# Kernel tuning notes

Hardware: AMD Instinct MI355X
Metric: run time of the kernel (lower is better)

Reference implementation:

```python
import jax, jax.numpy as jnp
import numpy as np

DIMS = [1024, 1024, 1024, 512]
BATCH = 1024
BETA = 1e-3
N_ITER = 20
LR_STATE = 0.5


def setup_inputs() -> dict:
    key = jax.random.key(0)
    ks = jax.random.split(key, 2 + len(DIMS) - 1)
    x = jax.random.normal(ks[0], (BATCH, DIMS[0]), dtype=jnp.float32)
    y = jax.random.normal(ks[1], (BATCH, DIMS[-1]), dtype=jnp.float32)
    inp = {"x": x, "y": y}
    # Weights: torch used randn*0.1; at these dims that makes the lr_state=0.5
    # gradient relaxation numerically unstable (Hessian I + W W^T has spectral
    # norm >> 2). We use a spectrally-normalized scale 0.5/sqrt(d_in) so the
    # fixed-point iteration is stable; the math of the module is unchanged.
    for i, (d_in, d_out) in enumerate(zip(DIMS[:-1], DIMS[1:])):
        inp[f"W{i}"] = jax.random.normal(ks[2 + i], (d_in, d_out), dtype=jnp.float32) * (0.5 / np.sqrt(d_in))
    return inp


def _forward_chain(x, Ws):
    # states[k+1] = states[k] @ W_k  -> the exact fixed point of the free energy
    states = [x]
    for W in Ws:
        states.append(states[-1] @ W)
    return states


def _state_grads(states, Ws, beta, y, coupled):
    """dE/ds_k for k=1..L (E = 0.5*sum ||s_{k+1} - s_k W_k||^2 + beta*0.5||s_L - y||^2).

    coupled=True reproduces torch's FIRST relaxation step, where states[1:]
    are still graph-connected via s_{k+1} = s_k @ W_k, so gradients also flow
    along that chain (g_total[k] = g_direct[k] + g_total[k+1] @ W_k^T).
    Later steps treat states as detached leaves (direct partials only).
    """
    L = len(Ws)
    g = []
    for k in range(1, L + 1):
        gk = states[k] - states[k - 1] @ Ws[k - 1]          # target side of term k-1
        if k < L:
            gk = gk - (states[k + 1] - states[k] @ Ws[k]) @ Ws[k].T  # pred side of term k
        else:
            gk = gk + beta * (states[k] - y)                 # clamp term
        g.append(gk)
    if coupled:
        for i in range(L - 2, -1, -1):
            g[i] = g[i] + g[i + 1] @ Ws[i + 1].T
    return g


def _relax_clamped(x, y, Ws, beta, n_iter, lr):
    states = _forward_chain(x, Ws)
    for it in range(n_iter):
        g = _state_grads(states, Ws, beta, y, coupled=(it == 0))
        states = [states[0]] + [s - lr * gk for s, gk in zip(states[1:], g)]
    return states


def _weight_grads(states, Ws):
    # dE/dW_i = s_i^T (s_i W_i - s_{i+1})
    return [states[i].T @ (states[i] @ W - states[i + 1]) for i, W in enumerate(Ws)]


def reference(x, y, W0, W1, W2):
    Ws = [W0, W1, W2]
    # Free phase (beta=0): the initial chain is the exact fixed point -- every
    # residual s_{k+1} - s_k W_k is bitwise zero, so all 20 torch relaxation
    # steps are exact no-ops. s0 is therefore just the forward chain.
    s0 = _forward_chain(x, Ws)
    # Weakly clamped phase.
    sb = _relax_clamped(x, y, Ws, BETA, N_ITER, LR_STATE)
    g0 = _weight_grads(s0, Ws)   # exactly zero at the free fixed point
    gb = _weight_grads(sb, Ws)
    ep_grads = [(b - a) / BETA for b, a in zip(gb, g0)]
    loss = jnp.mean((s0[-1] - y) ** 2)
    # Flatten EP weight grads + scalar loss into one vector output.
    return jnp.concatenate([g.ravel() for g in ep_grads] + [loss[None]])
```

## Files before the change

### kernel.cpp

```cpp
#include <hip/hip_runtime.h>


typedef float f32x4 __attribute__((ext_vector_type(4)));
typedef __bf16 bf16x8 __attribute__((ext_vector_type(8)));
typedef unsigned short u16;
typedef unsigned int u32;

namespace {

constexpr float LR = 0.5f;
constexpr float BETA = 1e-3f;

__device__ inline void splitbf(float v, u16& h, u16& l) {
  __bf16 hb = (__bf16)v;
  float hf = (float)hb;
  __bf16 lb = (__bf16)(v - hf);
  h = __builtin_bit_cast(u16, hb);
  l = __builtin_bit_cast(u16, lb);
}
__device__ inline u32 pack2(u16 a, u16 b) { return (u32)a | ((u32)b << 16); }

__device__ inline f32x4 MF(bf16x8 a, bf16x8 b, f32x4 c) {
  return __builtin_amdgcn_mfma_f32_16x16x32_bf16(a, b, c, 0, 0, 0);
}

__device__ inline int swzc(int row, int col) {
  return (col & ~63) | ((((col >> 3) & 7) ^ (row & 7)) << 3) | (col & 7);
}

struct GemmP {
  const u16 *Ah, *Al, *Bh, *Bl;
  const float *E0, *E1;
  float *of, *of2, *of3;
  u16 *oh, *ol;
  float alpha, c0, c1v;
  int N, K, ntn, role;
};

template <int NP>
__global__ __launch_bounds__(256) void gemm_g(GemmP ca, GemmP cb, GemmP cc,
                                              int nb0, int nb01) {
  constexpr int NARR = NP + 1;
  constexpr int NCH = NARR * 2;
  __shared__ u16 lds[2][NARR][64 * 64];
  GemmP c;
  int b = blockIdx.x;
  if (b < nb0) c = ca;
  else if (b < nb01) { c = cb; b -= nb0; }
  else { c = cc; b -= nb01; }
  const int tm = b / c.ntn, tn = b % c.ntn;
  const int tid = threadIdx.x, lane = tid & 63, w = tid >> 6;
  const int K = c.K;

  const char* gq[NCH];
  int loff[NCH];
  {
    const u16* bases[4] = {c.Ah, c.Al, c.Bh, c.Bl};
#pragma unroll
    for (int q = 0; q < NCH; ++q) {
      const int kb = q * 4 + w;
      const int a = kb >> 3, rb = kb & 7;
      const int row0 = (a < 2 ? tm : tn) << 6;
      gq[q] = (const char*)bases[a] +
              (((size_t)(row0 + rb * 8 + (lane >> 3)) * K) << 1) +
              ((lane & 7) << 4);
      loff[q] = a * 8192 + rb * 1024;
    }
  }

  const int wm = (w >> 1) << 5, wn = (w & 1) << 5;
  const int fr = lane & 15, fs = lane >> 4;
  int aoff[2][2], boff[2][2];
#pragma unroll
  for (int i = 0; i < 2; ++i)
#pragma unroll
    for (int kk = 0; kk < 2; ++kk) {
      const int ra = wm + i * 16 + fr;
      aoff[i][kk] = ra * 128 + ((((kk << 2) + fs) ^ (ra & 7)) << 4);
      const int rb2 = wn + i * 16 + fr;
      boff[i][kk] = rb2 * 128 + ((((kk << 2) + fs) ^ (rb2 & 7)) << 4);
    }

  auto stage = [&](int s, int buf) {
    char* lb = (char*)&lds[buf][0][0];
#pragma unroll
    for (int q = 0; q < NCH; ++q)
      __builtin_amdgcn_global_load_lds(
          (const __attribute__((address_space(1))) unsigned int*)(gq[q] +
                                                                  (size_t)s * 128),
          (__attribute__((address_space(3))) unsigned int*)(lb + loff[q]), 16,
          0, 0);
  };

  f32x4 acc[2][2] = {};
  const int nk = K >> 6;

  stage(0, 0);
  __syncthreads();
  int cur = 0;
  for (int s = 0; s < nk; ++s) {
    if (s + 1 < nk) stage(s + 1, cur ^ 1);
    const char* rb = (const char*)&lds[cur][0][0];
    bf16x8 ah[2][2], al[2][2], bh[2][2], bl[2][2];
#pragma unroll
    for (int i = 0; i < 2; ++i)
#pragma unroll
      for (int kk = 0; kk < 2; ++kk) {
        ah[i][kk] = *(const bf16x8*)(rb + aoff[i][kk]);
        al[i][kk] = *(const bf16x8*)(rb + 8192 + aoff[i][kk]);
        bh[i][kk] = *(const bf16x8*)(rb + 16384 + boff[i][kk]);
        if (NP == 3) bl[i][kk] = *(const bf16x8*)(rb + 24576 + boff[i][kk]);
      }
#pragma unroll
    for (int kk = 0; kk < 2; ++kk)
#pragma unroll
      for (int i = 0; i < 2; ++i)
#pragma unroll
        for (int j = 0; j < 2; ++j) {
          acc[i][j] = MF(ah[i][kk], bh[j][kk], acc[i][j]);
          acc[i][j] = MF(al[i][kk], bh[j][kk], acc[i][j]);
          if (NP == 3) acc[i][j] = MF(ah[i][kk], bl[j][kk], acc[i][j]);
        }
    __syncthreads();
    cur ^= 1;
  }

  const int N = c.N;
#pragma unroll
  for (int i = 0; i < 2; ++i)
#pragma unroll
    for (int j = 0; j < 2; ++j)
#pragma unroll
      for (int r = 0; r < 4; ++r) {
        const int gm = (tm << 6) + wm + i * 16 + (fs << 2) + r;
        const int gn = (tn << 6) + wn + j * 16 + fr;
        const size_t idx = (size_t)gm * N + gn;
        const size_t sidx = (size_t)gm * N + swzc(gm, gn);
        const float t = acc[i][j][r];
        if (c.role == 0) {
          float v = c.alpha * t;
          if (c.E0) v = fmaf(c.c0, c.E0[idx], v);
          if (c.E1) v = fmaf(c.c1v, c.E1[idx], v);
          if (c.of) c.of[idx] = v;
          if (c.oh) {
            u16 h, l;
            splitbf(v, h, l);
            c.oh[sidx] = h;
            c.ol[sidx] = l;
          }
        } else if (c.role == 1) {
          c.of[idx] = t;
          const float e = BETA * (t - c.E0[idx]);
          c.of2[idx] = e;
          u16 h, l;
          splitbf(e, h, l);
          c.oh[sidx] = h;
          c.ol[sidx] = l;
          c.of3[idx] = -LR * e;
        } else {
          const float d3o = c.E0[idx];
          const float r3 = d3o - t;
          u16 h, l;
          splitbf(r3, h, l);
          c.oh[sidx] = h;
          c.ol[sidx] = l;
          c.of[idx] = (1.0f - LR * BETA) * d3o - LR * r3 - LR * c.E1[idx];
        }
      }
}

template <bool WLO>
__global__ void split_s(const float* __restrict__ src, u16* __restrict__ oh,
                        u16* __restrict__ ol, int ngrp, int cshift) {
  const int g = blockIdx.x * blockDim.x + threadIdx.x;
  if (g >= ngrp) return;
  const int i = g * 8;
  const int r = i >> cshift;
  const int ci = i & ((1 << cshift) - 1);
  const float4 a = *(const float4*)(src + i);
  const float4 b = *(const float4*)(src + i + 4);
  const float v[8] = {a.x, a.y, a.z, a.w, b.x, b.y, b.z, b.w};
  u16 h[8], l[8];
#pragma unroll
  for (int j = 0; j < 8; ++j) splitbf(v[j], h[j], l[j]);
  const size_t dst = ((size_t)r << cshift) + (ci & ~63) +
                     ((((ci >> 3) & 7) ^ (r & 7)) << 3);
  *(uint4*)(oh + dst) = make_uint4(pack2(h[0], h[1]), pack2(h[2], h[3]),
                                   pack2(h[4], h[5]), pack2(h[6], h[7]));
  if (WLO)
    *(uint4*)(ol + dst) = make_uint4(pack2(l[0], l[1]), pack2(l[2], l[3]),
                                     pack2(l[4], l[5]), pack2(l[6], l[7]));
}

template <int OP>
__global__ __launch_bounds__(256) void split_t(const float* __restrict__ a,
                                               const float* __restrict__ b,
                                               u16* __restrict__ oh,
                                               u16* __restrict__ ol, int R,
                                               int C) {
  __shared__ float tile[64][65];
  const int tid = threadIdx.x;
  const int c0 = blockIdx.x << 6, r0 = blockIdx.y << 6;
#pragma unroll
  for (int q = 0; q < 16; ++q) {
    const int i = q * 256 + tid;
    const int r = i >> 6, cc = i & 63;
    const size_t src = (size_t)(r0 + r) * C + c0 + cc;
    float v = a[src];
    if (OP == 1) v += b[src];
    tile[r][cc] = v;
  }
  __syncthreads();
#pragma unroll
  for (int q = 0; q < 2; ++q) {
    const int g = q * 256 + tid;
    const int oc = g >> 3, os = g & 7;
    u16 h[8], l[8];
#pragma unroll
    for (int j = 0; j < 8; ++j) splitbf(tile[os * 8 + j][oc], h[j], l[j]);
    const int orow = c0 + oc;
    const size_t dst = (size_t)orow * R + r0 + ((os ^ (orow & 7)) << 3);
    *(uint4*)(oh + dst) = make_uint4(pack2(h[0], h[1]), pack2(h[2], h[3]),
                                     pack2(h[4], h[5]), pack2(h[6], h[7]));
    *(uint4*)(ol + dst) = make_uint4(pack2(l[0], l[1]), pack2(l[2], l[3]),
                                     pack2(l[4], l[5]), pack2(l[6], l[7]));
  }
}

__global__ void loss_sq(const float* __restrict__ e, float* __restrict__ partials,
                        int n) {
  __shared__ float red[256];
  float s = 0.f;
  for (int i = blockIdx.x * 256 + threadIdx.x; i < n; i += gridDim.x * 256)
    s = fmaf(e[i], e[i], s);
  red[threadIdx.x] = s;
  __syncthreads();
  for (int off = 128; off > 0; off >>= 1) {
    if (threadIdx.x < off) red[threadIdx.x] += red[threadIdx.x + off];
    __syncthreads();
  }
  if (threadIdx.x == 0) partials[blockIdx.x] = red[0];
}

__global__ void loss_final(const float* __restrict__ partials,
                           float* __restrict__ o, int np, float inv) {
  __shared__ float red[256];
  float s = 0.f;
  for (int i = threadIdx.x; i < np; i += 256) s += partials[i];
  red[threadIdx.x] = s;
  __syncthreads();
  for (int off = 128; off > 0; off >>= 1) {
    if (threadIdx.x < off) red[threadIdx.x] += red[threadIdx.x + off];
    __syncthreads();
  }
  if (threadIdx.x == 0) o[0] = red[0] * inv;
}

}

extern "C" void kernel_launch(void* const* d_in, const int* in_sizes, int n_in,
                              void* d_out, int out_size, void* d_ws, size_t ws_size,
                              hipStream_t stream) {
  const float* x  = (const float*)d_in[0];
  const float* y  = (const float*)d_in[1];
  const float* W0 = (const float*)d_in[2];
  const float* W1 = (const float*)d_in[3];
  const float* W2 = (const float*)d_in[4];
  float* out = (float*)d_out;

  const size_t M1 = 1u << 20;
  const size_t M5 = 1u << 19;

  char* wp = (char*)d_ws;
  auto F = [&](size_t n) { float* p = (float*)wp; wp += n * 4; return p; };
  auto U = [&](size_t n) { u16* p = (u16*)wp; wp += n * 2; return p; };

  float* c1 = F(M1);  float* c2 = F(M1);  float* c3 = F(M5);
  float* e3 = F(M5);  float* d1 = F(M1);  float* d2 = F(M1);
  float* d3 = F(M5);  float* r2f = F(M1); float* r3f = F(M5);
  float* lp = F(1024);

  u16* xh = U(M1);   u16* xl = U(M1);
  u16* xth = U(M1);  u16* xtl = U(M1);
  u16* W0th = U(M1); u16* W0tl = U(M1);
  u16* W1h = U(M1);
  u16* W1th = U(M1); u16* W1tl = U(M1);
  u16* W2h = U(M5);
  u16* W2th = U(M5); u16* W2tl = U(M5);
  u16* c1h = U(M1);  u16* c1l = U(M1);
  u16* c2h = U(M1);  u16* c2l = U(M1);
  u16* d1h = U(M1);  u16* d1l = U(M1);
  u16* d2h = U(M1);  u16* d2l = U(M1);
  u16* e3h = U(M5);  u16* e3l = U(M5);
  u16* r2h = U(M1);  u16* r2l = U(M1);
  u16* r3h = U(M5);  u16* r3l = U(M5);

  float* ep0 = out;
  float* ep1 = out + M1;
  float* ep2 = out + 2 * M1;
  float* lossp = out + 2 * M1 + M5;

  const dim3 blk(256);
  const float IB = -1.0f / BETA;

  auto mk = [](const u16* Ah, const u16* Al, const u16* Bh, const u16* Bl,
               int N, int K, int role, float alpha, float c0, float c1v,
               const float* E0, const float* E1, float* of, u16* oh, u16* ol,
               float* of2, float* of3) {
    GemmP p;
    p.Ah = Ah; p.Al = Al; p.Bh = Bh; p.Bl = Bl;
    p.E0 = E0; p.E1 = E1; p.of = of; p.of2 = of2; p.of3 = of3;
    p.oh = oh; p.ol = ol; p.alpha = alpha; p.c0 = c0; p.c1v = c1v;
    p.N = N; p.K = K; p.ntn = N >> 6; p.role = role;
    return p;
  };

  split_s<true><<<512, blk, 0, stream>>>(x, xh, xl, (int)(M1 / 8), 10);
  split_s<false><<<512, blk, 0, stream>>>(W1, W1h, nullptr, (int)(M1 / 8), 10);
  split_s<false><<<256, blk, 0, stream>>>(W2, W2h, nullptr, (int)(M5 / 8), 9);
  split_t<0><<<dim3(16, 16), blk, 0, stream>>>(x, nullptr, xth, xtl, 1024, 1024);
  split_t<0><<<dim3(16, 16), blk, 0, stream>>>(W0, nullptr, W0th, W0tl, 1024, 1024);
  split_t<0><<<dim3(16, 16), blk, 0, stream>>>(W1, nullptr, W1th, W1tl, 1024, 1024);
  split_t<0><<<dim3(8, 16), blk, 0, stream>>>(W2, nullptr, W2th, W2tl, 1024, 512);

  {
    GemmP p = mk(xh, xl, W0th, W0tl, 1024, 1024, 0, 1.f, 0.f, 0.f,
                 nullptr, nullptr, c1, c1h, c1l, nullptr, nullptr);
    gemm_g<3><<<256, blk, 0, stream>>>(p, p, p, 256, 256);
  }
  {
    GemmP p = mk(c1h, c1l, W1th, W1tl, 1024, 1024, 0, 1.f, 0.f, 0.f,
                 nullptr, nullptr, c2, c2h, c2l, nullptr, nullptr);
    gemm_g<3><<<256, blk, 0, stream>>>(p, p, p, 256, 256);
  }
  {
    GemmP p = mk(c2h, c2l, W2th, W2tl, 512, 1024, 1, 1.f, 0.f, 0.f,
                 y, nullptr, c3, e3h, e3l, e3, d3);
    gemm_g<3><<<128, blk, 0, stream>>>(p, p, p, 128, 128);
  }
  loss_sq<<<512, blk, 0, stream>>>(e3, lp, (int)M5);
  loss_final<<<1, blk, 0, stream>>>(lp, lossp, 512,
                                    1.0f / (BETA * BETA * (float)M5));

  {
    GemmP p = mk(e3h, e3l, W2h, nullptr, 1024, 512, 0, -LR, 0.f, 0.f,
                 nullptr, nullptr, d2, d2h, d2l, nullptr, nullptr);
    gemm_g<2><<<256, blk, 0, stream>>>(p, p, p, 256, 256);
  }
  {
    GemmP p = mk(d2h, d2l, W1h, nullptr, 1024, 1024, 0, 1.f, 0.f, 0.f,
                 nullptr, nullptr, d1, d1h, d1l, nullptr, nullptr);
    gemm_g<2><<<256, blk, 0, stream>>>(p, p, p, 256, 256);
  }

  for (int it = 1; it < 20; ++it) {
    GemmP pa = mk(d1h, d1l, W1th, nullptr, 1024, 1024, 0, -1.f, 1.f, 0.f,
                  d2, nullptr, r2f, r2h, r2l, nullptr, nullptr);
    GemmP pb = mk(d2h, d2l, W2th, nullptr, 512, 1024, 2, 0.f, 0.f, 0.f,
                  d3, e3, d3, r3h, r3l, nullptr, nullptr);
    gemm_g<2><<<384, blk, 0, stream>>>(pa, pb, pb, 256, 384);
    GemmP pc = mk(r2h, r2l, W1h, nullptr, 1024, 1024, 0, LR, 1.f - LR, 0.f,
                  d1, nullptr, d1, d1h, d1l, nullptr, nullptr);
    GemmP pd = mk(r3h, r3l, W2h, nullptr, 1024, 512, 0, LR, 1.f, -LR,
                  d2, r2f, d2, d2h, d2l, nullptr, nullptr);
    gemm_g<2><<<512, blk, 0, stream>>>(pc, pd, pd, 256, 512);
  }

  {
    GemmP pa = mk(d1h, d1l, W1th, nullptr, 1024, 1024, 0, -1.f, 1.f, 0.f,
                  d2, nullptr, r2f, nullptr, nullptr, nullptr, nullptr);
    GemmP pb = mk(d2h, d2l, W2th, nullptr, 512, 1024, 0, -1.f, 1.f, 0.f,
                  d3, nullptr, r3f, nullptr, nullptr, nullptr, nullptr);
    gemm_g<2><<<384, blk, 0, stream>>>(pa, pb, pb, 256, 384);
  }

  u16 *s1th = c1h, *s1tl = c1l, *s2th = c2h, *s2tl = c2l;
  u16 *r1th = W0th, *r1tl = W0tl, *r2th = xh, *r2tl = xl;
  u16 *r3th = e3h, *r3tl = e3l;
  split_t<1><<<dim3(16, 16), blk, 0, stream>>>(c1, d1, s1th, s1tl, 1024, 1024);
  split_t<1><<<dim3(16, 16), blk, 0, stream>>>(c2, d2, s2th, s2tl, 1024, 1024);
  split_t<0><<<dim3(16, 16), blk, 0, stream>>>(d1, nullptr, r1th, r1tl, 1024, 1024);
  split_t<0><<<dim3(16, 16), blk, 0, stream>>>(r2f, nullptr, r2th, r2tl, 1024, 1024);
  split_t<0><<<dim3(8, 16), blk, 0, stream>>>(r3f, nullptr, r3th, r3tl, 1024, 512);

  {
    GemmP p0 = mk(xth, xtl, r1th, r1tl, 1024, 1024, 0, IB, 0.f, 0.f,
                  nullptr, nullptr, ep0, nullptr, nullptr, nullptr, nullptr);
    GemmP p1 = mk(s1th, s1tl, r2th, r2tl, 1024, 1024, 0, IB, 0.f, 0.f,
                  nullptr, nullptr, ep1, nullptr, nullptr, nullptr, nullptr);
    GemmP p2 = mk(s2th, s2tl, r3th, r3tl, 512, 1024, 0, IB, 0.f, 0.f,
                  nullptr, nullptr, ep2, nullptr, nullptr, nullptr, nullptr);
    gemm_g<3><<<640, blk, 0, stream>>>(p0, p1, p2, 256, 512);
  }
}
```

Measured before the change: 988.0 us.

## Precompute Gram matrices to halve relaxation launches and fuse split kernels

The relaxation is reformulated so each iteration updates d1, d2, d3 directly in one launch. It uses precomputed products W1·W1^T, W2·W2^T and W1·W2 (G1, G2, P), with multi-region K concatenation in the GEMM and ping-pong buffers. This replaces the two dependent launches per iteration (residual then update) with one, and merges the split/transpose and initial GEMMs into fewer multi-config launches. The cost is extra precompute GEMMs and longer K loops per tile. The Gram terms are stored only as a bf16 hi part, which may reduce accuracy.

```diff
diff --git a/kernel.cpp b/kernel.cpp
--- a/kernel.cpp
+++ b/kernel.cpp
@@ -28,44 +28,46 @@
   return (col & ~63) | ((((col >> 3) & 7) ^ (row & 7)) << 3) | (col & 7);
 }
 
+struct Region {
+  const u16 *Ah, *Al, *Bh, *Bl;
+  int kw, nks;
+};
+
 struct GemmP {
-  const u16 *Ah, *Al, *Bh, *Bl;
+  Region rg[3];
   const float *E0, *E1;
   float *of, *of2, *of3;
-  u16 *oh, *ol;
+  u16 *oh, *ol, *oh2, *ol2;
   float alpha, c0, c1v;
-  int N, K, ntn, role;
+  int N, ntn, role;
 };
 
 template <int NP>
 __global__ __launch_bounds__(256) void gemm_g(GemmP ca, GemmP cb, GemmP cc,
-                                              int nb0, int nb01) {
+                                              GemmP cd, int nb0, int nb1,
+                                              int nb2) {
   constexpr int NARR = NP + 1;
   constexpr int NCH = NARR * 2;
   __shared__ u16 lds[2][NARR][64 * 64];
   GemmP c;
   int b = blockIdx.x;
   if (b < nb0) c = ca;
-  else if (b < nb01) { c = cb; b -= nb0; }
-  else { c = cc; b -= nb01; }
+  else if (b < nb1) { c = cb; b -= nb0; }
+  else if (b < nb2) { c = cc; b -= nb1; }
+  else { c = cd; b -= nb2; }
   const int tm = b / c.ntn, tn = b % c.ntn;
   const int tid = threadIdx.x, lane = tid & 63, w = tid >> 6;
-  const int K = c.K;
-
-  const char* gq[NCH];
-  int loff[NCH];
-  {
-    const u16* bases[4] = {c.Ah, c.Al, c.Bh, c.Bl};
-#pragma unroll
-    for (int q = 0; q < NCH; ++q) {
-      const int kb = q * 4 + w;
-      const int a = kb >> 3, rb = kb & 7;
-      const int row0 = (a < 2 ? tm : tn) << 6;
-      gq[q] = (const char*)bases[a] +
-              (((size_t)(row0 + rb * 8 + (lane >> 3)) * K) << 1) +
-              ((lane & 7) << 4);
-      loff[q] = a * 8192 + rb * 1024;
-    }
+
+  const int inrow = (lane & 7) << 4;
+  int ro2048[NCH], ro1024[NCH], loffq[NCH];
+#pragma unroll
+  for (int q = 0; q < NCH; ++q) {
+    const int a = q >> 1;
+    const int rb = (q & 1) * 4 + w;
+    const int row = ((a < 2) ? tm : tn) * 64 + rb * 8 + (lane >> 3);
+    ro2048[q] = row * 2048 + inrow;
+    ro1024[q] = row * 1024 + inrow;
+    loffq[q] = a * 8192 + rb * 1024;
   }
 
   const int wm = (w >> 1) << 5, wn = (w & 1) << 5;
@@ -81,20 +83,31 @@
       boff[i][kk] = rb2 * 128 + ((((kk << 2) + fs) ^ (rb2 & 7)) << 4);
     }
 
+  const int rs1 = c.rg[0].nks;
+  const int rs2 = rs1 + c.rg[1].nks;
+  const int nk = rs2 + c.rg[2].nks;
+
   auto stage = [&](int s, int buf) {
+    const int r = (s >= rs1) + (s >= rs2);
+    const Region& rg = (r == 0) ? c.rg[0] : (r == 1) ? c.rg[1] : c.rg[2];
+    const int local = s - ((r == 0) ? 0 : (r == 1) ? rs1 : rs2);
+    const bool wide = (rg.kw == 1024);
     char* lb = (char*)&lds[buf][0][0];
 #pragma unroll
-    for (int q = 0; q < NCH; ++q)
+    for (int q = 0; q < NCH; ++q) {
+      const int a = q >> 1;
+      const u16* base = (a == 0) ? rg.Ah : (a == 1) ? rg.Al
+                        : (a == 2) ? rg.Bh : rg.Bl;
+      const char* src = (const char*)base + (wide ? ro2048[q] : ro1024[q]) +
+                        (size_t)local * 128;
       __builtin_amdgcn_global_load_lds(
-          (const __attribute__((address_space(1))) unsigned int*)(gq[q] +
-                                                                  (size_t)s * 128),
-          (__attribute__((address_space(3))) unsigned int*)(lb + loff[q]), 16,
+          (const __attribute__((address_space(1))) unsigned int*)src,
+          (__attribute__((address_space(3))) unsigned int*)(lb + loffq[q]), 16,
           0, 0);
+    }
   };
 
   f32x4 acc[2][2] = {};
-  const int nk = K >> 6;
-
   stage(0, 0);
   __syncthreads();
   int cur = 0;
@@ -146,68 +159,80 @@
             u16 h, l;
             splitbf(v, h, l);
             c.oh[sidx] = h;
-            c.ol[sidx] = l;
+            if (c.ol) c.ol[sidx] = l;
           }
-        } else if (c.role == 1) {
-          c.of[idx] = t;
+        } else {
           const float e = BETA * (t - c.E0[idx]);
           c.of2[idx] = e;
           u16 h, l;
           splitbf(e, h, l);
           c.oh[sidx] = h;
           c.ol[sidx] = l;
-          c.of3[idx] = -LR * e;
-        } else {
-          const float d3o = c.E0[idx];
-          const float r3 = d3o - t;
-          u16 h, l;
-          splitbf(r3, h, l);
-          c.oh[sidx] = h;
-          c.ol[sidx] = l;
-          c.of[idx] = (1.0f - LR * BETA) * d3o - LR * r3 - LR * c.E1[idx];
+          const float dv = -LR * e;
+          c.of3[idx] = dv;
+          splitbf(dv, h, l);
+          c.oh2[sidx] = h;
+          c.ol2[sidx] = l;
         }
       }
 }
 
-template <bool WLO>
-__global__ void split_s(const float* __restrict__ src, u16* __restrict__ oh,
-                        u16* __restrict__ ol, int ngrp, int cshift) {
-  const int g = blockIdx.x * blockDim.x + threadIdx.x;
-  if (g >= ngrp) return;
+struct SCfg {
+  const float* src;
+  u16 *oh, *ol;
+  int nblk, cshift;
+};
+
+__global__ void split_s_m(SCfg ca, SCfg cb, SCfg cc, int nb0, int nb1) {
+  SCfg c;
+  int b = blockIdx.x;
+  if (b < nb0) c = ca;
+  else if (b < nb1) { c = cb; b -= nb0; }
+  else { c = cc; b -= nb1; }
+  const int g = b * 256 + threadIdx.x;
   const int i = g * 8;
-  const int r = i >> cshift;
-  const int ci = i & ((1 << cshift) - 1);
-  const float4 a = *(const float4*)(src + i);
-  const float4 b = *(const float4*)(src + i + 4);
-  const float v[8] = {a.x, a.y, a.z, a.w, b.x, b.y, b.z, b.w};
+  const int r = i >> c.cshift;
+  const int ci = i & ((1 << c.cshift) - 1);
+  const float4 a = *(const float4*)(c.src + i);
+  const float4 b4 = *(const float4*)(c.src + i + 4);
+  const float v[8] = {a.x, a.y, a.z, a.w, b4.x, b4.y, b4.z, b4.w};
   u16 h[8], l[8];
 #pragma unroll
   for (int j = 0; j < 8; ++j) splitbf(v[j], h[j], l[j]);
-  const size_t dst = ((size_t)r << cshift) + (ci & ~63) +
+  const size_t dst = ((size_t)r << c.cshift) + (ci & ~63) +
                      ((((ci >> 3) & 7) ^ (r & 7)) << 3);
-  *(uint4*)(oh + dst) = make_uint4(pack2(h[0], h[1]), pack2(h[2], h[3]),
-                                   pack2(h[4], h[5]), pack2(h[6], h[7]));
-  if (WLO)
-    *(uint4*)(ol + dst) = make_uint4(pack2(l[0], l[1]), pack2(l[2], l[3]),
-                                     pack2(l[4], l[5]), pack2(l[6], l[7]));
-}
-
-template <int OP>
-__global__ __launch_bounds__(256) void split_t(const float* __restrict__ a,
-                                               const float* __restrict__ b,
-                                               u16* __restrict__ oh,
-                                               u16* __restrict__ ol, int R,
-                                               int C) {
+  *(uint4*)(c.oh + dst) = make_uint4(pack2(h[0], h[1]), pack2(h[2], h[3]),
+                                     pack2(h[4], h[5]), pack2(h[6], h[7]));
+  if (c.ol)
+    *(uint4*)(c.ol + dst) = make_uint4(pack2(l[0], l[1]), pack2(l[2], l[3]),
+                                       pack2(l[4], l[5]), pack2(l[6], l[7]));
+}
+
+struct TCfg {
+  const float *a, *b;
+  u16 *oh, *ol;
+  int R, C, nbx, op;
+};
+
+__global__ __launch_bounds__(256) void split_t_m(TCfg c0, TCfg c1, TCfg c2,
+                                                 TCfg c3, TCfg c4, int4 nb) {
   __shared__ float tile[64][65];
+  TCfg c;
+  int b = blockIdx.x;
+  if (b < nb.x) c = c0;
+  else if (b < nb.y) { c = c1; b -= nb.x; }
+  else if (b < nb.z) { c = c2; b -= nb.y; }
+  else if (b < nb.w) { c = c3; b -= nb.z; }
+  else { c = c4; b -= nb.w; }
   const int tid = threadIdx.x;
-  const int c0 = blockIdx.x << 6, r0 = blockIdx.y << 6;
+  const int cb0 = (b % c.nbx) << 6, r0 = (b / c.nbx) << 6;
 #pragma unroll
   for (int q = 0; q < 16; ++q) {
     const int i = q * 256 + tid;
     const int r = i >> 6, cc = i & 63;
-    const size_t src = (size_t)(r0 + r) * C + c0 + cc;
-    float v = a[src];
-    if (OP == 1) v += b[src];
+    const size_t src = (size_t)(r0 + r) * c.C + cb0 + cc;
+    float v = c.a[src];
+    if (c.op == 1) v += c.b[src];
     tile[r][cc] = v;
   }
   __syncthreads();
@@ -218,12 +243,12 @@
     u16 h[8], l[8];
 #pragma unroll
     for (int j = 0; j < 8; ++j) splitbf(tile[os * 8 + j][oc], h[j], l[j]);
-    const int orow = c0 + oc;
-    const size_t dst = (size_t)orow * R + r0 + ((os ^ (orow & 7)) << 3);
-    *(uint4*)(oh + dst) = make_uint4(pack2(h[0], h[1]), pack2(h[2], h[3]),
-                                     pack2(h[4], h[5]), pack2(h[6], h[7]));
-    *(uint4*)(ol + dst) = make_uint4(pack2(l[0], l[1]), pack2(l[2], l[3]),
-                                     pack2(l[4], l[5]), pack2(l[6], l[7]));
+    const int orow = cb0 + oc;
+    const size_t dst = (size_t)orow * c.R + r0 + ((os ^ (orow & 7)) << 3);
+    *(uint4*)(c.oh + dst) = make_uint4(pack2(h[0], h[1]), pack2(h[2], h[3]),
+                                       pack2(h[4], h[5]), pack2(h[6], h[7]));
+    *(uint4*)(c.ol + dst) = make_uint4(pack2(l[0], l[1]), pack2(l[2], l[3]),
+                                       pack2(l[4], l[5]), pack2(l[6], l[7]));
   }
 }
 
@@ -275,25 +300,35 @@
   auto F = [&](size_t n) { float* p = (float*)wp; wp += n * 4; return p; };
   auto U = [&](size_t n) { u16* p = (u16*)wp; wp += n * 2; return p; };
 
-  float* c1 = F(M1);  float* c2 = F(M1);  float* c3 = F(M5);
-  float* e3 = F(M5);  float* d1 = F(M1);  float* d2 = F(M1);
-  float* d3 = F(M5);  float* r2f = F(M1); float* r3f = F(M5);
+  float* c1f = F(M1);
+  float* c2f = F(M1);
+  float* e3f = F(M5);
+  float* d1f[2] = {F(M1), F(M1)};
+  float* d2f[2] = {F(M1), F(M1)};
+  float* d3f[2] = {F(M5), F(M5)};
+  float* r2f = F(M1);
+  float* r3f = F(M5);
   float* lp = F(1024);
 
-  u16* xh = U(M1);   u16* xl = U(M1);
-  u16* xth = U(M1);  u16* xtl = U(M1);
-  u16* W0th = U(M1); u16* W0tl = U(M1);
-  u16* W1h = U(M1);
-  u16* W1th = U(M1); u16* W1tl = U(M1);
-  u16* W2h = U(M5);
-  u16* W2th = U(M5); u16* W2tl = U(M5);
-  u16* c1h = U(M1);  u16* c1l = U(M1);
-  u16* c2h = U(M1);  u16* c2l = U(M1);
-  u16* d1h = U(M1);  u16* d1l = U(M1);
-  u16* d2h = U(M1);  u16* d2l = U(M1);
-  u16* e3h = U(M5);  u16* e3l = U(M5);
-  u16* r2h = U(M1);  u16* r2l = U(M1);
-  u16* r3h = U(M5);  u16* r3l = U(M5);
+  u16 *xh = U(M1), *xl = U(M1);
+  u16 *xth = U(M1), *xtl = U(M1);
+  u16 *W0th = U(M1), *W0tl = U(M1);
+  u16 *W1h = U(M1), *W1l = U(M1);
+  u16 *W1th = U(M1), *W1tl = U(M1);
+  u16 *W2h = U(M5), *W2l = U(M5);
+  u16 *W2th = U(M5), *W2tl = U(M5);
+  u16 *G1h = U(M1), *G2h = U(M1), *Ph = U(M5);
+  u16 *c1h = U(M1), *c1l = U(M1);
+  u16 *c2h = U(M1), *c2l = U(M1);
+  u16 *e3h = U(M5), *e3l = U(M5);
+  u16 *d1h[2] = {U(M1), U(M1)}, *d1l[2] = {U(M1), U(M1)};
+  u16 *d2h[2] = {U(M1), U(M1)}, *d2l[2] = {U(M1), U(M1)};
+  u16 *d3h[2] = {U(M5), U(M5)}, *d3l[2] = {U(M5), U(M5)};
+  u16 *s1th = U(M1), *s1tl = U(M1);
+  u16 *s2th = U(M1), *s2tl = U(M1);
+  u16 *r1th = U(M1), *r1tl = U(M1);
+  u16 *r2th = U(M1), *r2tl = U(M1);
+  u16 *r3th = U(M5), *r3tl = U(M5);
 
   float* ep0 = out;
   float* ep1 = out + M1;
@@ -303,93 +338,114 @@
   const dim3 blk(256);
   const float IB = -1.0f / BETA;
 
-  auto mk = [](const u16* Ah, const u16* Al, const u16* Bh, const u16* Bl,
-               int N, int K, int role, float alpha, float c0, float c1v,
-               const float* E0, const float* E1, float* of, u16* oh, u16* ol,
-               float* of2, float* of3) {
-    GemmP p;
-    p.Ah = Ah; p.Al = Al; p.Bh = Bh; p.Bl = Bl;
-    p.E0 = E0; p.E1 = E1; p.of = of; p.of2 = of2; p.of3 = of3;
-    p.oh = oh; p.ol = ol; p.alpha = alpha; p.c0 = c0; p.c1v = c1v;
-    p.N = N; p.K = K; p.ntn = N >> 6; p.role = role;
+  auto R = [](const u16* ah, const u16* al, const u16* bh, const u16* bl,
+              int kw) {
+    Region r;
+    r.Ah = ah; r.Al = al; r.Bh = bh; r.Bl = bl;
+    r.kw = kw; r.nks = kw >> 6;
+    return r;
+  };
+  auto mk = [&](Region r0, float alpha, int N, const float* E0,
+                const float* E1, float c0, float c1v, float* of, u16* oh,
+                u16* ol) {
+    GemmP p{};
+    p.rg[0] = r0;
+    p.rg[1] = r0; p.rg[1].nks = 0;
+    p.rg[2] = r0; p.rg[2].nks = 0;
+    p.E0 = E0; p.E1 = E1;
+    p.of = of; p.of2 = nullptr; p.of3 = nullptr;
+    p.oh = oh; p.ol = ol; p.oh2 = nullptr; p.ol2 = nullptr;
+    p.alpha = alpha; p.c0 = c0; p.c1v = c1v;
+    p.N = N; p.ntn = N >> 6; p.role = 0;
     return p;
   };
 
-  split_s<true><<<512, blk, 0, stream>>>(x, xh, xl, (int)(M1 / 8), 10);
-  split_s<false><<<512, blk, 0, stream>>>(W1, W1h, nullptr, (int)(M1 / 8), 10);
-  split_s<false><<<256, blk, 0, stream>>>(W2, W2h, nullptr, (int)(M5 / 8), 9);
-  split_t<0><<<dim3(16, 16), blk, 0, stream>>>(x, nullptr, xth, xtl, 1024, 1024);
-  split_t<0><<<dim3(16, 16), blk, 0, stream>>>(W0, nullptr, W0th, W0tl, 1024, 1024);
-  split_t<0><<<dim3(16, 16), blk, 0, stream>>>(W1, nullptr, W1th, W1tl, 1024, 1024);
-  split_t<0><<<dim3(8, 16), blk, 0, stream>>>(W2, nullptr, W2th, W2tl, 1024, 512);
-
-  {
-    GemmP p = mk(xh, xl, W0th, W0tl, 1024, 1024, 0, 1.f, 0.f, 0.f,
-                 nullptr, nullptr, c1, c1h, c1l, nullptr, nullptr);
-    gemm_g<3><<<256, blk, 0, stream>>>(p, p, p, 256, 256);
-  }
-  {
-    GemmP p = mk(c1h, c1l, W1th, W1tl, 1024, 1024, 0, 1.f, 0.f, 0.f,
-                 nullptr, nullptr, c2, c2h, c2l, nullptr, nullptr);
-    gemm_g<3><<<256, blk, 0, stream>>>(p, p, p, 256, 256);
-  }
-  {
-    GemmP p = mk(c2h, c2l, W2th, W2tl, 512, 1024, 1, 1.f, 0.f, 0.f,
-                 y, nullptr, c3, e3h, e3l, e3, d3);
-    gemm_g<3><<<128, blk, 0, stream>>>(p, p, p, 128, 128);
-  }
-  loss_sq<<<512, blk, 0, stream>>>(e3, lp, (int)M5);
+  {
+    SCfg a{x, xh, xl, 512, 10};
+    SCfg b{W1, W1h, W1l, 512, 10};
+    SCfg c{W2, W2h, W2l, 256, 9};
+    split_s_m<<<1280, blk, 0, stream>>>(a, b, c, 512, 1024);
+  }
+  {
+    TCfg t0{x, nullptr, xth, xtl, 1024, 1024, 16, 0};
+    TCfg t1{W0, nullptr, W0th, W0tl, 1024, 1024, 16, 0};
+    TCfg t2{W1, nullptr, W1th, W1tl, 1024, 1024, 16, 0};
+    TCfg t3{W2, nullptr, W2th, W2tl, 1024, 512, 8, 0};
+    split_t_m<<<896, blk, 0, stream>>>(t0, t1, t2, t3, t3,
+                                       make_int4(256, 512, 768, 896));
+  }
+  {
+    GemmP g1 = mk(R(W1h, W1l, W1h, W1l, 1024), -1.f, 1024, nullptr, nullptr,
+                  0.f, 0.f, nullptr, G1h, nullptr);
+    GemmP g2 = mk(R(W2h, W2l, W2h, W2l, 512), -1.f, 1024, nullptr, nullptr,
+                  0.f, 0.f, nullptr, G2h, nullptr);
+    GemmP pp = mk(R(W1h, W1l, W2th, W2tl, 1024), 1.f, 512, nullptr, nullptr,
+                  0.f, 0.f, nullptr, Ph, nullptr);
+    GemmP c1 = mk(R(xh, xl, W0th, W0tl, 1024), 1.f, 1024, nullptr, nullptr,
+                  0.f, 0.f, c1f, c1h, c1l);
+    gemm_g<3><<<896, blk, 0, stream>>>(g1, g2, pp, c1, 256, 512, 640);
+  }
+  {
+    GemmP c2 = mk(R(c1h, c1l, W1th, W1tl, 1024), 1.f, 1024, nullptr, nullptr,
+                  0.f, 0.f, c2f, c2h, c2l);
+    gemm_g<3><<<256, blk, 0, stream>>>(c2, c2, c2, c2, 256, 256, 256);
+  }
+  {
+    GemmP p = mk(R(c2h, c2l, W2th, W2tl, 1024), 1.f, 512, y, nullptr, 0.f,
+                 0.f, nullptr, e3h, e3l);
+    p.role = 1;
+    p.of2 = e3f;
+    p.of3 = d3f[0];
+    p.oh2 = d3h[0];
+    p.ol2 = d3l[0];
+    gemm_g<3><<<128, blk, 0, stream>>>(p, p, p, p, 128, 128, 128);
+  }
+  {
+    GemmP pd2 = mk(R(e3h, e3l, W2h, nullptr, 512), -LR, 1024, nullptr,
+                   nullptr, 0.f, 0.f, d2f[0], d2h[0], d2l[0]);
+    GemmP pd1 = mk(R(e3h, e3l, Ph, nullptr, 512), -LR, 1024, nullptr, nullptr,
+                   0.f, 0.f, d1f[0], d1h[0], d1l[0]);
+    gemm_g<2><<<512, blk, 0, stream>>>(pd2, pd1, pd1, pd1, 256, 512, 512);
+  }
+  for (int t = 1; t < 20; ++t) {
+    const int sp = (t - 1) & 1, dp = t & 1;
+    GemmP A = mk(R(d2h[sp], d2l[sp], W1h, nullptr, 1024), LR, 1024, d1f[sp],
+                 nullptr, 1.f - LR, 0.f, d1f[dp], d1h[dp], d1l[dp]);
+    A.rg[1] = R(d1h[sp], d1l[sp], G1h, nullptr, 1024);
+    GemmP B = mk(R(d1h[sp], d1l[sp], W1th, nullptr, 1024), LR, 1024, d2f[sp],
+                 nullptr, 1.f - LR, 0.f, d2f[dp], d2h[dp], d2l[dp]);
+    B.rg[1] = R(d3h[sp], d3l[sp], W2h, nullptr, 512);
+    B.rg[2] = R(d2h[sp], d2l[sp], G2h, nullptr, 1024);
+    GemmP C = mk(R(d2h[sp], d2l[sp], W2th, nullptr, 1024), LR, 512, d3f[sp],
+                 e3f, 1.f - LR - LR * BETA, -LR, d3f[dp], d3h[dp], d3l[dp]);
+    gemm_g<2><<<640, blk, 0, stream>>>(A, B, C, C, 256, 512, 640);
+  }
+  {
+    GemmP p2 = mk(R(d1h[1], d1l[1], W1th, nullptr, 1024), -1.f, 1024, d2f[1],
+                  nullptr, 1.f, 0.f, r2f, nullptr, nullptr);
+    GemmP p3 = mk(R(d2h[1], d2l[1], W2th, nullptr, 1024), -1.f, 512, d3f[1],
+                  nullptr, 1.f, 0.f, r3f, nullptr, nullptr);
+    gemm_g<2><<<384, blk, 0, stream>>>(p2, p3, p3, p3, 256, 384, 384);
+  }
+  {
+    TCfg t0{c1f, d1f[1], s1th, s1tl, 1024, 1024, 16, 1};
+    TCfg t1{c2f, d2f[1], s2th, s2tl, 1024, 1024, 16, 1};
+    TCfg t2{d1f[1], nullptr, r1th, r1tl, 1024, 1024, 16, 0};
+    TCfg t3{r2f, nullptr, r2th, r2tl, 1024, 1024, 16, 0};
+    TCfg t4{r3f, nullptr, r3th, r3tl, 1024, 512, 8, 0};
+    split_t_m<<<1152, blk, 0, stream>>>(t0, t1, t2, t3, t4,
+                                        make_int4(256, 512, 768, 1024));
+  }
+  {
+    GemmP p0 = mk(R(xth, xtl, r1th, r1tl, 1024), IB, 1024, nullptr, nullptr,
+                  0.f, 0.f, ep0, nullptr, nullptr);
+    GemmP p1 = mk(R(s1th, s1tl, r2th, r2tl, 1024), IB, 1024, nullptr, nullptr,
+                  0.f, 0.f, ep1, nullptr, nullptr);
+    GemmP p2 = mk(R(s2th, s2tl, r3th, r3tl, 1024), IB, 512, nullptr, nullptr,
+                  0.f, 0.f, ep2, nullptr, nullptr);
+    gemm_g<3><<<640, blk, 0, stream>>>(p0, p1, p2, p2, 256, 512, 640);
+  }
+  loss_sq<<<512, blk, 0, stream>>>(e3f, lp, (int)M5);
   loss_final<<<1, blk, 0, stream>>>(lp, lossp, 512,
                                     1.0f / (BETA * BETA * (float)M5));
-
-  {
-    GemmP p = mk(e3h, e3l, W2h, nullptr, 1024, 512, 0, -LR, 0.f, 0.f,
-                 nullptr, nullptr, d2, d2h, d2l, nullptr, nullptr);
-    gemm_g<2><<<256, blk, 0, stream>>>(p, p, p, 256, 256);
-  }
-  {
-    GemmP p = mk(d2h, d2l, W1h, nullptr, 1024, 1024, 0, 1.f, 0.f, 0.f,
-                 nullptr, nullptr, d1, d1h, d1l, nullptr, nullptr);
-    gemm_g<2><<<256, blk, 0, stream>>>(p, p, p, 256, 256);
-  }
-
-  for (int it = 1; it < 20; ++it) {
-    GemmP pa = mk(d1h, d1l, W1th, nullptr, 1024, 1024, 0, -1.f, 1.f, 0.f,
-                  d2, nullptr, r2f, r2h, r2l, nullptr, nullptr);
-    GemmP pb = mk(d2h, d2l, W2th, nullptr, 512, 1024, 2, 0.f, 0.f, 0.f,
-                  d3, e3, d3, r3h, r3l, nullptr, nullptr);
-    gemm_g<2><<<384, blk, 0, stream>>>(pa, pb, pb, 256, 384);
-    GemmP pc = mk(r2h, r2l, W1h, nullptr, 1024, 1024, 0, LR, 1.f - LR, 0.f,
-                  d1, nullptr, d1, d1h, d1l, nullptr, nullptr);
-    GemmP pd = mk(r3h, r3l, W2h, nullptr, 1024, 512, 0, LR, 1.f, -LR,
-                  d2, r2f, d2, d2h, d2l, nullptr, nullptr);
-    gemm_g<2><<<512, blk, 0, stream>>>(pc, pd, pd, 256, 512);
-  }
-
-  {
-    GemmP pa = mk(d1h, d1l, W1th, nullptr, 1024, 1024, 0, -1.f, 1.f, 0.f,
-                  d2, nullptr, r2f, nullptr, nullptr, nullptr, nullptr);
-    GemmP pb = mk(d2h, d2l, W2th, nullptr, 512, 1024, 0, -1.f, 1.f, 0.f,
-                  d3, nullptr, r3f, nullptr, nullptr, nullptr, nullptr);
-    gemm_g<2><<<384, blk, 0, stream>>>(pa, pb, pb, 256, 384);
-  }
-
-  u16 *s1th = c1h, *s1tl = c1l, *s2th = c2h, *s2tl = c2l;
-  u16 *r1th = W0th, *r1tl = W0tl, *r2th = xh, *r2tl = xl;
-  u16 *r3th = e3h, *r3tl = e3l;
-  split_t<1><<<dim3(16, 16), blk, 0, stream>>>(c1, d1, s1th, s1tl, 1024, 1024);
-  split_t<1><<<dim3(16, 16), blk, 0, stream>>>(c2, d2, s2th, s2tl, 1024, 1024);
-  split_t<0><<<dim3(16, 16), blk, 0, stream>>>(d1, nullptr, r1th, r1tl, 1024, 1024);
-  split_t<0><<<dim3(16, 16), blk, 0, stream>>>(r2f, nullptr, r2th, r2tl, 1024, 1024);
-  split_t<0><<<dim3(8, 16), blk, 0, stream>>>(r3f, nullptr, r3th, r3tl, 1024, 512);
-
-  {
-    GemmP p0 = mk(xth, xtl, r1th, r1tl, 1024, 1024, 0, IB, 0.f, 0.f,
-                  nullptr, nullptr, ep0, nullptr, nullptr, nullptr, nullptr);
-    GemmP p1 = mk(s1th, s1tl, r2th, r2tl, 1024, 1024, 0, IB, 0.f, 0.f,
-                  nullptr, nullptr, ep1, nullptr, nullptr, nullptr, nullptr);
-    GemmP p2 = mk(s2th, s2tl, r3th, r3tl, 512, 1024, 0, IB, 0.f, 0.f,
-                  nullptr, nullptr, ep2, nullptr, nullptr, nullptr, nullptr);
-    gemm_g<3><<<640, blk, 0, stream>>>(p0, p1, p2, 256, 512);
-  }
-}
+}
```

After: 1.583 ms. 1.6x slower.
